# Kernel tuning notes

Measured on AMD Instinct MI355X. Metric: run time of the kernel, lower is better.

Reference implementation:

```python
import jax, jax.numpy as jnp
import numpy as np

B, L, H2 = 64, 1024, 1024  # batch, src_len, 2*hidden_size


def setup_inputs() -> dict:
    key = jax.random.key(0)
    k1, k2, k3, k4, k5, k6 = jax.random.split(key, 6)
    s = 0.02
    return {
        "s_t_hat": jax.random.normal(k1, (B, H2), jnp.float32),
        "encoder_outputs": jax.random.normal(k2, (B, L, H2), jnp.float32),
        "encoder_features": jax.random.normal(k3, (B * L, H2), jnp.float32),
        "encoder_pad_mask": jnp.ones((B, L), jnp.float32),
        "W": jax.random.normal(k4, (H2, H2), jnp.float32) * s,  # W_s_b_attn.weight
        "b": jax.random.normal(k5, (H2,), jnp.float32) * s,     # W_s_b_attn.bias
        "v": jax.random.normal(k6, (H2,), jnp.float32) * s,     # v.weight (no bias)
    }


def reference(s_t_hat, encoder_outputs, encoder_features, encoder_pad_mask, W, b, v):
    Bb, Ll, Hh = encoder_outputs.shape
    # decoder_features = W_s_b_attn(s_t_hat), broadcast over src positions
    dec = s_t_hat @ W.T + b                                # [B, H2]
    attn_feats = encoder_features.reshape(Bb, Ll, Hh) + dec[:, None, :]
    e = jnp.tanh(attn_feats) @ v                            # [B, L]
    attn_dist = jax.nn.softmax(e, axis=1) * encoder_pad_mask
    attn_dist = attn_dist / attn_dist.sum(axis=1, keepdims=True)
    c_t = jnp.einsum('bl,blh->bh', attn_dist, encoder_outputs)  # [B, H2]
    return c_t
```

## Files before the change

### kernel.cpp

```cpp
#include <hip/hip_runtime.h>

#define H2    1024
#define LSRC  1024
#define BATCH 64

__device__ __forceinline__ float fast_tanh(float x) {
  float e2 = __expf(2.0f * x);
  return 1.0f - 2.0f / (e2 + 1.0f);
}

__global__ __launch_bounds__(256) void dec_kernel(
    const float* __restrict__ s, const float* __restrict__ W,
    const float* __restrict__ bias, float* __restrict__ dec) {
  const int KT = 128;
  __shared__ float s_lds[BATCH][KT + 1];
  __shared__ float w_lds[16][KT];
  const int t  = threadIdx.x;
  const int h0 = blockIdx.x * 16;
  const int bi = t & 63;
  const int hg = t >> 6;
  float acc[4] = {0.f, 0.f, 0.f, 0.f};
  for (int k0 = 0; k0 < H2; k0 += KT) {
    __syncthreads();
    for (int idx = t; idx < BATCH * KT; idx += 256) {
      int r = idx >> 7, c = idx & (KT - 1);
      s_lds[r][c] = s[r * H2 + k0 + c];
    }
    for (int idx = t; idx < 16 * KT; idx += 256) {
      int r = idx >> 7, c = idx & (KT - 1);
      w_lds[r][c] = W[(h0 + r) * H2 + k0 + c];
    }
    __syncthreads();
    for (int k = 0; k < KT; ++k) {
      float sv = s_lds[bi][k];
#pragma unroll
      for (int j = 0; j < 4; ++j) acc[j] += sv * w_lds[hg + 4 * j][k];
    }
  }
#pragma unroll
  for (int j = 0; j < 4; ++j) {
    int h = h0 + hg + 4 * j;
    dec[bi * H2 + h] = acc[j] + bias[h];
  }
}

__global__ __launch_bounds__(256) void e_kernel(
    const float* __restrict__ ef, const float* __restrict__ dec,
    const float* __restrict__ v, float* __restrict__ e) {
  const int lane = threadIdx.x & 63;
  const int wave = threadIdx.x >> 6;
  const int row  = blockIdx.x * 4 + wave;
  const int b    = row >> 10;
  const float4* ef4  = (const float4*)(ef) + (size_t)row * 256;
  const float4* dec4 = (const float4*)(dec) + (size_t)b * 256;
  const float4* v4   = (const float4*)(v);
  float sum = 0.f;
#pragma unroll
  for (int i = 0; i < 4; ++i) {
    int idx = lane + 64 * i;
    float4 x  = ef4[idx];
    float4 d  = dec4[idx];
    float4 vv = v4[idx];
    sum += fast_tanh(x.x + d.x) * vv.x;
    sum += fast_tanh(x.y + d.y) * vv.y;
    sum += fast_tanh(x.z + d.z) * vv.z;
    sum += fast_tanh(x.w + d.w) * vv.w;
  }
#pragma unroll
  for (int off = 32; off; off >>= 1) sum += __shfl_xor(sum, off);
  if (lane == 0) e[row] = sum;
}

__global__ __launch_bounds__(256) void softmax_kernel(
    const float* __restrict__ e, const float* __restrict__ mask,
    float* __restrict__ attn) {
  __shared__ float wmax[4], wsum[4];
  const int b = blockIdx.x, t = threadIdx.x;
  const int lane = t & 63, wave = t >> 6;
  float4 ev = ((const float4*)(e + b * LSRC))[t];
  float4 mk = ((const float4*)(mask + b * LSRC))[t];
  float m = fmaxf(fmaxf(ev.x, ev.y), fmaxf(ev.z, ev.w));
#pragma unroll
  for (int off = 32; off; off >>= 1) m = fmaxf(m, __shfl_xor(m, off));
  if (lane == 0) wmax[wave] = m;
  __syncthreads();
  m = fmaxf(fmaxf(wmax[0], wmax[1]), fmaxf(wmax[2], wmax[3]));
  float e0 = __expf(ev.x - m) * mk.x;
  float e1 = __expf(ev.y - m) * mk.y;
  float e2 = __expf(ev.z - m) * mk.z;
  float e3 = __expf(ev.w - m) * mk.w;
  float ssum = e0 + e1 + e2 + e3;
#pragma unroll
  for (int off = 32; off; off >>= 1) ssum += __shfl_xor(ssum, off);
  if (lane == 0) wsum[wave] = ssum;
  __syncthreads();
  float inv = 1.0f / (wsum[0] + wsum[1] + wsum[2] + wsum[3]);
  float4 o = {e0 * inv, e1 * inv, e2 * inv, e3 * inv};
  ((float4*)(attn + b * LSRC))[t] = o;
}

__global__ __launch_bounds__(256) void ct_partial_kernel(
    const float* __restrict__ attn, const float* __restrict__ eo,
    float* __restrict__ part) {
  const int lc = blockIdx.x;
  const int b  = blockIdx.y;
  const int t  = threadIdx.x;
  const float*  ab  = attn + b * LSRC;
  const float4* eob = (const float4*)(eo) + (size_t)b * LSRC * 256;
  float4 acc = {0.f, 0.f, 0.f, 0.f};
  const int l0 = lc * (LSRC / 8);
#pragma unroll 4
  for (int l = l0; l < l0 + LSRC / 8; ++l) {
    float  a = ab[l];
    float4 x = eob[(size_t)l * 256 + t];
    acc.x += a * x.x; acc.y += a * x.y; acc.z += a * x.z; acc.w += a * x.w;
  }
  ((float4*)(part) + (size_t)(lc * BATCH + b) * 256)[t] = acc;
}

__global__ __launch_bounds__(256) void reduce_kernel(
    const float* __restrict__ part, float* __restrict__ out) {
  const int b = blockIdx.x, t = threadIdx.x;
  float4 s = {0.f, 0.f, 0.f, 0.f};
#pragma unroll
  for (int lc = 0; lc < 8; ++lc) {
    float4 x = ((const float4*)(part) + (size_t)(lc * BATCH + b) * 256)[t];
    s.x += x.x; s.y += x.y; s.z += x.z; s.w += x.w;
  }
  ((float4*)(out) + (size_t)b * 256)[t] = s;
}

extern "C" void kernel_launch(void* const* d_in, const int* in_sizes, int n_in,
                              void* d_out, int out_size, void* d_ws, size_t ws_size,
                              hipStream_t stream) {
  const float* s_t_hat  = (const float*)d_in[0];
  const float* enc_out  = (const float*)d_in[1];
  const float* enc_feat = (const float*)d_in[2];
  const float* mask     = (const float*)d_in[3];
  const float* W        = (const float*)d_in[4];
  const float* bias     = (const float*)d_in[5];
  const float* v        = (const float*)d_in[6];
  float* out = (float*)d_out;

  float* dec  = (float*)d_ws;
  float* e    = dec  + BATCH * H2;
  float* attn = e    + BATCH * LSRC;
  float* part = attn + BATCH * LSRC;

  dec_kernel<<<H2 / 16, 256, 0, stream>>>(s_t_hat, W, bias, dec);
  e_kernel<<<(BATCH * LSRC) / 4, 256, 0, stream>>>(enc_feat, dec, v, e);
  softmax_kernel<<<BATCH, 256, 0, stream>>>(e, mask, attn);
  ct_partial_kernel<<<dim3(8, BATCH), 256, 0, stream>>>(attn, enc_out, part);
  reduce_kernel<<<BATCH, 256, 0, stream>>>(part, out);
}
```

Measured before the change: 152.9 us.

## Vectorize dec GEMV, batch e rows per block, split c_t over more chunks

The dec kernel now loads and reads LDS with float4, and the e kernel keeps the dec and v vectors in registers while each wave processes 8 rows. tanh uses a hardware reciprocal instead of a divide. The c_t partial kernel stages attention weights in LDS and splits L into 16 or 32 chunks when the workspace is large enough, which gives more blocks for the 256MB stream. The trade-off is more partial-sum traffic in the reduce step and slightly lower tanh precision.

```diff
diff --git a/kernel.cpp b/kernel.cpp
--- a/kernel.cpp
+++ b/kernel.cpp
@@ -6,42 +6,48 @@
 
 __device__ __forceinline__ float fast_tanh(float x) {
   float e2 = __expf(2.0f * x);
-  return 1.0f - 2.0f / (e2 + 1.0f);
+  return 1.0f - 2.0f * __builtin_amdgcn_rcpf(e2 + 1.0f);
 }
 
 __global__ __launch_bounds__(256) void dec_kernel(
     const float* __restrict__ s, const float* __restrict__ W,
     const float* __restrict__ bias, float* __restrict__ dec) {
-  const int KT = 128;
-  __shared__ float s_lds[BATCH][KT + 1];
-  __shared__ float w_lds[16][KT];
+  __shared__ float s_lds[BATCH][132];
+  __shared__ float w_lds[16][128];
   const int t  = threadIdx.x;
   const int h0 = blockIdx.x * 16;
   const int bi = t & 63;
   const int hg = t >> 6;
-  float acc[4] = {0.f, 0.f, 0.f, 0.f};
-  for (int k0 = 0; k0 < H2; k0 += KT) {
+  float4 acc = {0.f, 0.f, 0.f, 0.f};
+  for (int k0 = 0; k0 < H2; k0 += 128) {
     __syncthreads();
-    for (int idx = t; idx < BATCH * KT; idx += 256) {
-      int r = idx >> 7, c = idx & (KT - 1);
-      s_lds[r][c] = s[r * H2 + k0 + c];
+    for (int idx = t; idx < BATCH * 32; idx += 256) {
+      int r = idx >> 5, c = idx & 31;
+      float4 x = ((const float4*)(s + (size_t)r * H2 + k0))[c];
+      *(float4*)&s_lds[r][c * 4] = x;
     }
-    for (int idx = t; idx < 16 * KT; idx += 256) {
-      int r = idx >> 7, c = idx & (KT - 1);
-      w_lds[r][c] = W[(h0 + r) * H2 + k0 + c];
+    for (int idx = t; idx < 16 * 32; idx += 256) {
+      int r = idx >> 5, c = idx & 31;
+      float4 x = ((const float4*)(W + (size_t)(h0 + r) * H2 + k0))[c];
+      *(float4*)&w_lds[r][c * 4] = x;
     }
     __syncthreads();
-    for (int k = 0; k < KT; ++k) {
-      float sv = s_lds[bi][k];
-#pragma unroll
-      for (int j = 0; j < 4; ++j) acc[j] += sv * w_lds[hg + 4 * j][k];
+    for (int kq = 0; kq < 32; ++kq) {
+      float4 sv = *(const float4*)&s_lds[bi][kq * 4];
+      float4 w0 = *(const float4*)&w_lds[hg][kq * 4];
+      float4 w1 = *(const float4*)&w_lds[hg + 4][kq * 4];
+      float4 w2 = *(const float4*)&w_lds[hg + 8][kq * 4];
+      float4 w3 = *(const float4*)&w_lds[hg + 12][kq * 4];
+      acc.x += sv.x * w0.x + sv.y * w0.y + sv.z * w0.z + sv.w * w0.w;
+      acc.y += sv.x * w1.x + sv.y * w1.y + sv.z * w1.z + sv.w * w1.w;
+      acc.z += sv.x * w2.x + sv.y * w2.y + sv.z * w2.z + sv.w * w2.w;
+      acc.w += sv.x * w3.x + sv.y * w3.y + sv.z * w3.z + sv.w * w3.w;
     }
   }
-#pragma unroll
-  for (int j = 0; j < 4; ++j) {
-    int h = h0 + hg + 4 * j;
-    dec[bi * H2 + h] = acc[j] + bias[h];
-  }
+  dec[bi * H2 + h0 + hg]      = acc.x + bias[h0 + hg];
+  dec[bi * H2 + h0 + hg + 4]  = acc.y + bias[h0 + hg + 4];
+  dec[bi * H2 + h0 + hg + 8]  = acc.z + bias[h0 + hg + 8];
+  dec[bi * H2 + h0 + hg + 12] = acc.w + bias[h0 + hg + 12];
 }
 
 __global__ __launch_bounds__(256) void e_kernel(
@@ -49,26 +55,34 @@
     const float* __restrict__ v, float* __restrict__ e) {
   const int lane = threadIdx.x & 63;
   const int wave = threadIdx.x >> 6;
-  const int row  = blockIdx.x * 4 + wave;
-  const int b    = row >> 10;
-  const float4* ef4  = (const float4*)(ef) + (size_t)row * 256;
+  const int b    = blockIdx.x >> 5;
+  const int r0   = (blockIdx.x & 31) * 32;
   const float4* dec4 = (const float4*)(dec) + (size_t)b * 256;
   const float4* v4   = (const float4*)(v);
-  float sum = 0.f;
+  float4 d[4], vv[4];
 #pragma unroll
-  for (int i = 0; i < 4; ++i) {
-    int idx = lane + 64 * i;
-    float4 x  = ef4[idx];
-    float4 d  = dec4[idx];
-    float4 vv = v4[idx];
-    sum += fast_tanh(x.x + d.x) * vv.x;
-    sum += fast_tanh(x.y + d.y) * vv.y;
-    sum += fast_tanh(x.z + d.z) * vv.z;
-    sum += fast_tanh(x.w + d.w) * vv.w;
+  for (int j = 0; j < 4; ++j) {
+    d[j]  = dec4[lane + 64 * j];
+    vv[j] = v4[lane + 64 * j];
   }
+  const float4* efb = (const float4*)(ef) + ((size_t)b * LSRC + r0) * 256;
 #pragma unroll
-  for (int off = 32; off; off >>= 1) sum += __shfl_xor(sum, off);
-  if (lane == 0) e[row] = sum;
+  for (int i = 0; i < 8; ++i) {
+    int rl = wave + 4 * i;
+    const float4* row = efb + (size_t)rl * 256;
+    float sum = 0.f;
+#pragma unroll
+    for (int j = 0; j < 4; ++j) {
+      float4 x = row[lane + 64 * j];
+      sum += fast_tanh(x.x + d[j].x) * vv[j].x;
+      sum += fast_tanh(x.y + d[j].y) * vv[j].y;
+      sum += fast_tanh(x.z + d[j].z) * vv[j].z;
+      sum += fast_tanh(x.w + d[j].w) * vv[j].w;
+    }
+#pragma unroll
+    for (int off = 32; off; off >>= 1) sum += __shfl_xor(sum, off);
+    if (lane == 0) e[b * LSRC + r0 + rl] = sum;
+  }
 }
 
 __global__ __launch_bounds__(256) void softmax_kernel(
@@ -101,17 +115,19 @@
 
 __global__ __launch_bounds__(256) void ct_partial_kernel(
     const float* __restrict__ attn, const float* __restrict__ eo,
-    float* __restrict__ part) {
+    float* __restrict__ part, int CH) {
+  __shared__ float a_lds[128];
   const int lc = blockIdx.x;
   const int b  = blockIdx.y;
   const int t  = threadIdx.x;
-  const float*  ab  = attn + b * LSRC;
-  const float4* eob = (const float4*)(eo) + (size_t)b * LSRC * 256;
+  const int l0 = lc * CH;
+  if (t < CH) a_lds[t] = attn[b * LSRC + l0 + t];
+  __syncthreads();
+  const float4* eob = (const float4*)(eo) + ((size_t)b * LSRC + l0) * 256;
   float4 acc = {0.f, 0.f, 0.f, 0.f};
-  const int l0 = lc * (LSRC / 8);
-#pragma unroll 4
-  for (int l = l0; l < l0 + LSRC / 8; ++l) {
-    float  a = ab[l];
+#pragma unroll 8
+  for (int l = 0; l < CH; ++l) {
+    float  a = a_lds[l];
     float4 x = eob[(size_t)l * 256 + t];
     acc.x += a * x.x; acc.y += a * x.y; acc.z += a * x.z; acc.w += a * x.w;
   }
@@ -119,11 +135,10 @@
 }
 
 __global__ __launch_bounds__(256) void reduce_kernel(
-    const float* __restrict__ part, float* __restrict__ out) {
+    const float* __restrict__ part, float* __restrict__ out, int nch) {
   const int b = blockIdx.x, t = threadIdx.x;
   float4 s = {0.f, 0.f, 0.f, 0.f};
-#pragma unroll
-  for (int lc = 0; lc < 8; ++lc) {
+  for (int lc = 0; lc < nch; ++lc) {
     float4 x = ((const float4*)(part) + (size_t)(lc * BATCH + b) * 256)[t];
     s.x += x.x; s.y += x.y; s.z += x.z; s.w += x.w;
   }
@@ -147,9 +162,16 @@
   float* attn = e    + BATCH * LSRC;
   float* part = attn + BATCH * LSRC;
 
+  const size_t base  = (size_t)3 * BATCH * H2 * sizeof(float);
+  const size_t chunk = (size_t)BATCH * H2 * sizeof(float);
+  int nch = 8;
+  if (ws_size >= base + 32 * chunk)      nch = 32;
+  else if (ws_size >= base + 16 * chunk) nch = 16;
+  const int CH = LSRC / nch;
+
   dec_kernel<<<H2 / 16, 256, 0, stream>>>(s_t_hat, W, bias, dec);
-  e_kernel<<<(BATCH * LSRC) / 4, 256, 0, stream>>>(enc_feat, dec, v, e);
+  e_kernel<<<BATCH * 32, 256, 0, stream>>>(enc_feat, dec, v, e);
   softmax_kernel<<<BATCH, 256, 0, stream>>>(e, mask, attn);
-  ct_partial_kernel<<<dim3(8, BATCH), 256, 0, stream>>>(attn, enc_out, part);
-  reduce_kernel<<<BATCH, 256, 0, stream>>>(part, out);
+  ct_partial_kernel<<<dim3(nch, BATCH), 256, 0, stream>>>(attn, enc_out, part, CH);
+  reduce_kernel<<<BATCH, 256, 0, stream>>>(part, out, nch);
 }
```

Result: slower. 158.3 us (+3.5%).
